# Optimization experiments

Measured on AMD Instinct MI355X. Metric: run time of the kernel, lower is better.

Reference implementation:

```python
import jax, jax.numpy as jnp
import numpy as np

N = 50000        # nodes
E = 800000       # edges (avg degree 16)
G = 64           # graphs in batch
F_IN = 9
OUT = 10


def setup_inputs() -> dict:
    key = jax.random.key(0)
    ks = jax.random.split(key, 20)
    def w(k, fi, fo):
        return jax.random.normal(k, (fi, fo), dtype=jnp.float32) * (1.0 / np.sqrt(fi))
    inp = {
        "x": jax.random.normal(ks[0], (N, F_IN), dtype=jnp.float32),
        "edge_index": jax.random.randint(ks[1], (2, E), 0, N, dtype=jnp.int64),
        "batch": jnp.sort(jax.random.randint(ks[2], (N,), 0, G, dtype=jnp.int64)),
        # GCNConv weights (PyG: x @ W then normalized scatter-add, + bias)
        "W1": w(ks[3], F_IN, 128), "b1": jnp.zeros((128,), jnp.float32),
        "W2": w(ks[4], 128, 256),  "b2": jnp.zeros((256,), jnp.float32),
        "W3": w(ks[5], 256, 256),  "b3": jnp.zeros((256,), jnp.float32),
        "W4": w(ks[6], 256, 256),  "b4": jnp.zeros((256,), jnp.float32),
        # dense head
        "Wl2": w(ks[7], 256, 128), "bl2": jnp.zeros((128,), jnp.float32),
        "Wl3": w(ks[8], 128, 128), "bl3": jnp.zeros((128,), jnp.float32),
        "Wl":  w(ks[9], 128, OUT), "bl":  jnp.zeros((OUT,), jnp.float32),
    }
    return inp


def reference(x, edge_index, batch, W1, b1, W2, b2, W3, b3, W4, b4,
              Wl2, bl2, Wl3, bl3, Wl, bl):
    # GCNConv with self-loops and symmetric deg^{-1/2} normalization
    loops = jnp.arange(N, dtype=edge_index.dtype)
    src = jnp.concatenate([edge_index[0], loops])   # [E+N]
    dst = jnp.concatenate([edge_index[1], loops])
    deg = jax.ops.segment_sum(jnp.ones_like(src, dtype=x.dtype), dst, num_segments=N)
    dinv = jax.lax.rsqrt(deg)                        # deg >= 1 due to self-loops
    norm = (dinv[src] * dinv[dst])[:, None]          # [E+N, 1]

    def conv(h, W, b):
        msg = (h @ W)[src] * norm                    # gather + normalize
        return jax.ops.segment_sum(msg, dst, num_segments=N) + b

    h = jax.nn.relu(conv(x, W1, b1))
    h = jax.nn.relu(conv(h, W2, b2))
    h = jax.nn.relu(conv(h, W3, b3))
    h = conv(h, W4, b4)                              # no relu before pool
    g = jax.ops.segment_max(h, batch, num_segments=G)  # global_max_pool -> [G, 256]
    g = jax.nn.relu(g @ Wl2 + bl2)
    g = jax.nn.relu(g @ Wl3 + bl3)
    out = g @ Wl + bl                                # [G, OUT]
    return jnp.squeeze(out)
```

## Files before the change

kernel.cpp:

```cpp
#include <hip/hip_runtime.h>
#include <float.h>

#define NN 50000
#define NE 800000
#define NG 64
#define CAP 64

typedef __attribute__((ext_vector_type(8))) short bf16x8;
typedef __attribute__((ext_vector_type(4))) float f32x4;
typedef __attribute__((ext_vector_type(4))) _Float16 half4;
typedef __attribute__((ext_vector_type(2))) _Float16 half2v;
typedef unsigned int u32;

__device__ __forceinline__ unsigned f2mono(float f) {
  unsigned b = __float_as_uint(f);
  return (b & 0x80000000u) ? ~b : (b | 0x80000000u);
}
__device__ __forceinline__ float mono2f(unsigned u) {
  unsigned b = (u & 0x80000000u) ? (u & 0x7fffffffu) : ~u;
  return __uint_as_float(b);
}
__device__ __forceinline__ unsigned short bf16rn(float f) {
  unsigned u = __float_as_uint(f);
  unsigned r = u + 0x7FFFu + ((u >> 16) & 1u);
  return (unsigned short)(r >> 16);
}
__device__ __forceinline__ float bf2f(unsigned short h) {
  return __uint_as_float(((unsigned)h) << 16);
}
__device__ __forceinline__ void split2(float a, unsigned short* hi, unsigned short* lo) {
  unsigned short h = bf16rn(a);
  *hi = h;
  *lo = bf16rn(a - bf2f(h));
}
__device__ __forceinline__ void gl_lds16(const void* g, void* l) {
  __builtin_amdgcn_global_load_lds((const __attribute__((address_space(1))) u32*)g,
                                   (__attribute__((address_space(3))) u32*)l, 16, 0, 0);
}

__global__ void k_count(const int* __restrict__ src, const int* __restrict__ dst,
                        int* __restrict__ cnt, int* __restrict__ col) {
  int e = blockIdx.x * blockDim.x + threadIdx.x;
  if (e >= NE) return;
  int d = dst[e];
  int s = src[e];
  if ((unsigned)d >= NN || (unsigned)s >= NN) return;
  int pos = atomicAdd(&cnt[d], 1);
  if (pos < CAP) col[d * CAP + pos] = s;
}

__global__ void k_dinv(const int* __restrict__ cnt, float* __restrict__ dinv,
                       const float* __restrict__ x, float* __restrict__ xs) {
  int v = blockIdx.x * blockDim.x + threadIdx.x;
  if (v >= NN) return;
  float d = rsqrtf((float)cnt[v] + 1.0f);
  dinv[v] = d;
#pragma unroll
  for (int i = 0; i < 9; ++i) xs[v * 9 + i] = x[v * 9 + i] * d;
}

__global__ void k_splitw(const float* __restrict__ W, unsigned short* __restrict__ Wi,
                         int K, int Nc) {
  int i = blockIdx.x * blockDim.x + threadIdx.x;
  if (i >= K * Nc) return;
  int k = i / Nc, n = i - k * Nc;
  float w = W[i];
  unsigned short h, l;
  split2(w, &h, &l);
  size_t base = (size_t)n * 2 * K + (size_t)(k >> 3) * 16 + (k & 7);
  Wi[base] = h;
  Wi[base + 8] = l;
}

__global__ __launch_bounds__(256) void k_agg9(const float* __restrict__ xs,
                                              float* __restrict__ out,
                                              const int* __restrict__ cnt,
                                              const int* __restrict__ col,
                                              const float* __restrict__ dinv) {
  int v = (blockIdx.x * 256 + threadIdx.x) >> 4;
  int l = threadIdx.x & 15;
  if (v >= NN) return;
  int c = cnt[v]; if (c > CAP) c = CAP;
  const int* cl = col + v * CAP;
  float acc = (l < 9) ? xs[v * 9 + l] : 0.0f;
  int j = 0;
  for (; j + 4 <= c; j += 4) {
    int4 u = *(const int4*)(cl + j);
    float a0 = (l < 9) ? xs[u.x * 9 + l] : 0.f;
    float a1 = (l < 9) ? xs[u.y * 9 + l] : 0.f;
    float a2 = (l < 9) ? xs[u.z * 9 + l] : 0.f;
    float a3 = (l < 9) ? xs[u.w * 9 + l] : 0.f;
    acc += (a0 + a1) + (a2 + a3);
  }
  for (; j < c; ++j) {
    int u = cl[j];
    if (l < 9) acc += xs[u * 9 + l];
  }
  if (l < 9) out[v * 9 + l] = acc * dinv[v];
}

__global__ __launch_bounds__(256) void k_gemm9(const float* __restrict__ in,
                                               const float* __restrict__ W,
                                               const float* __restrict__ bias,
                                               const float* __restrict__ dinv,
                                               _Float16* __restrict__ out) {
  __shared__ float sW[9 * 128];
  __shared__ float sb[128];
  int t = threadIdx.x;
  if (t < 128) sb[t] = bias[t];
  for (int i = t; i < 9 * 128; i += 256) sW[i] = W[i];
  __syncthreads();
  int r = blockIdx.x * 2 + (t >> 7);
  int c = t & 127;
  if (r >= NN) return;
  float acc = sb[c];
#pragma unroll
  for (int i = 0; i < 9; ++i) acc += in[r * 9 + i] * sW[i * 128 + c];
  out[r * 128 + c] = (_Float16)(fmaxf(acc, 0.0f) * dinv[r]);
}

__global__ __launch_bounds__(256) void k_agg128(const half2v* __restrict__ h,
                                                unsigned short* __restrict__ Ai,
                                                const int* __restrict__ cnt,
                                                const int* __restrict__ col,
                                                const float* __restrict__ dinv) {
  int w = (blockIdx.x * 256 + threadIdx.x) >> 6;
  int lane = threadIdx.x & 63;
  if (w >= NN) return;
  half2v s = h[(size_t)w * 64 + lane];
  float ax = (float)s.x, ay = (float)s.y;
  int c = cnt[w]; if (c > CAP) c = CAP;
  const int* cl = col + w * CAP;
  int j = 0;
  for (; j + 4 <= c; j += 4) {
    int4 u = *(const int4*)(cl + j);
    half2v t0 = h[(size_t)u.x * 64 + lane];
    half2v t1 = h[(size_t)u.y * 64 + lane];
    half2v t2 = h[(size_t)u.z * 64 + lane];
    half2v t3 = h[(size_t)u.w * 64 + lane];
    ax += ((float)t0.x + (float)t1.x) + ((float)t2.x + (float)t3.x);
    ay += ((float)t0.y + (float)t1.y) + ((float)t2.y + (float)t3.y);
  }
  for (; j < c; ++j) {
    int u = cl[j];
    half2v tv = h[(size_t)u * 64 + lane];
    ax += (float)tv.x; ay += (float)tv.y;
  }
  float di = dinv[w];
  ax *= di; ay *= di;
  ushort2 hv, lv;
  split2(ax, &hv.x, &lv.x);
  split2(ay, &hv.y, &lv.y);
  size_t base = (size_t)w * 256 + (size_t)(lane >> 2) * 16 + 2 * (lane & 3);
  *(ushort2*)(Ai + base) = hv;
  *(ushort2*)(Ai + base + 8) = lv;
}

__global__ __launch_bounds__(256) void k_agg256(const half4* __restrict__ h,
                                                unsigned short* __restrict__ Ai,
                                                const int* __restrict__ cnt,
                                                const int* __restrict__ col,
                                                const float* __restrict__ dinv) {
  int w = (blockIdx.x * 256 + threadIdx.x) >> 6;
  int lane = threadIdx.x & 63;
  if (w >= NN) return;
  half4 s = h[(size_t)w * 64 + lane];
  float ax = (float)s.x, ay = (float)s.y, az = (float)s.z, aw = (float)s.w;
  int c = cnt[w]; if (c > CAP) c = CAP;
  const int* cl = col + w * CAP;
  int j = 0;
  for (; j + 4 <= c; j += 4) {
    int4 u = *(const int4*)(cl + j);
    half4 t0 = h[(size_t)u.x * 64 + lane];
    half4 t1 = h[(size_t)u.y * 64 + lane];
    half4 t2 = h[(size_t)u.z * 64 + lane];
    half4 t3 = h[(size_t)u.w * 64 + lane];
    ax += ((float)t0.x + (float)t1.x) + ((float)t2.x + (float)t3.x);
    ay += ((float)t0.y + (float)t1.y) + ((float)t2.y + (float)t3.y);
    az += ((float)t0.z + (float)t1.z) + ((float)t2.z + (float)t3.z);
    aw += ((float)t0.w + (float)t1.w) + ((float)t2.w + (float)t3.w);
  }
  for (; j < c; ++j) {
    int u = cl[j];
    half4 tv = h[(size_t)u * 64 + lane];
    ax += (float)tv.x; ay += (float)tv.y; az += (float)tv.z; aw += (float)tv.w;
  }
  float di = dinv[w];
  ax *= di; ay *= di; az *= di; aw *= di;
  ushort4 hv, lv;
  split2(ax, &hv.x, &lv.x);
  split2(ay, &hv.y, &lv.y);
  split2(az, &hv.z, &lv.z);
  split2(aw, &hv.w, &lv.w);
  size_t base = (size_t)w * 512 + (size_t)(lane >> 1) * 16 + 4 * (lane & 1);
  *(ushort4*)(Ai + base) = hv;
  *(ushort4*)(Ai + base + 8) = lv;
}

__global__ __launch_bounds__(256) void k_mm(const unsigned short* __restrict__ A,
                                            const unsigned short* __restrict__ B,
                                            const float* __restrict__ bias,
                                            _Float16* __restrict__ C,
                                            const float* __restrict__ dinv,
                                            const int* __restrict__ batch,
                                            unsigned* __restrict__ gpool,
                                            int M, int K, int Nc, int mode) {
  __shared__ __align__(16) unsigned short Al[128 * 64];
  __shared__ __align__(16) unsigned short Bl[128 * 64];
  int t = threadIdx.x;
  int wave = t >> 6, lane = t & 63;
  int wm = wave & 1, wn = wave >> 1;
  int rowBase = blockIdx.x * 128;
  int colBase = blockIdx.y * 128;
  int lm = lane & 15;
  int q  = lane >> 4;
  unsigned K2 = 2u * (unsigned)K;

  int srl  = wave * 32 + (lane >> 3);
  int sj   = lane & 7;
  int ssw  = srl & 7;

  f32x4 acc[4][4];
#pragma unroll
  for (int i = 0; i < 4; ++i)
#pragma unroll
    for (int j = 0; j < 4; ++j) acc[i][j] = (f32x4){0.f, 0.f, 0.f, 0.f};

  int nsteps = K >> 5;
  for (int s = 0; s < nsteps; ++s) {
    __syncthreads();
#pragma unroll
    for (int c = 0; c < 4; ++c) {
      int rl = srl + c * 8;
      int gseg = s * 8 + (sj ^ ssw);
      int ga = rowBase + rl; if (ga > M - 1) ga = M - 1;
      gl_lds16(A + (size_t)ga * K2 + gseg * 8, Al + (wave * 32 + c * 8) * 64 + lane * 8);
      int gb = colBase + rl;
      gl_lds16(B + (size_t)gb * K2 + gseg * 8, Bl + (wave * 32 + c * 8) * 64 + lane * 8);
    }
    __syncthreads();

    bf16x8 bh[4], blv[4];
#pragma unroll
    for (int ni = 0; ni < 4; ++ni) {
      int r = wn * 64 + ni * 16 + lm;
      const unsigned short* p = Bl + r * 64;
      int sw = r & 7;
      bh[ni]  = *(const bf16x8*)(p + ((2 * q) ^ sw) * 8);
      blv[ni] = *(const bf16x8*)(p + ((2 * q + 1) ^ sw) * 8);
    }
#pragma unroll
    for (int mi = 0; mi < 4; ++mi) {
      int r = wm * 64 + mi * 16 + lm;
      const unsigned short* p = Al + r * 64;
      int sw = r & 7;
      bf16x8 ah = *(const bf16x8*)(p + ((2 * q) ^ sw) * 8);
      bf16x8 al = *(const bf16x8*)(p + ((2 * q + 1) ^ sw) * 8);
#pragma unroll
      for (int ni = 0; ni < 4; ++ni) {
        acc[mi][ni] = __builtin_amdgcn_mfma_f32_16x16x32_bf16(ah, bh[ni],  acc[mi][ni], 0, 0, 0);
        acc[mi][ni] = __builtin_amdgcn_mfma_f32_16x16x32_bf16(ah, blv[ni], acc[mi][ni], 0, 0, 0);
        acc[mi][ni] = __builtin_amdgcn_mfma_f32_16x16x32_bf16(al, bh[ni],  acc[mi][ni], 0, 0, 0);
      }
    }
  }

  int rowOff = (lane >> 4) * 4;
  if (mode == 2) {
    __syncthreads();
    unsigned* ldsPool = (unsigned*)Al;
    for (int i = t; i < 4 * 256; i += 256) ldsPool[i] = 0u;
    __syncthreads();
    int b0 = batch[rowBase];
#pragma unroll
    for (int mi = 0; mi < 4; ++mi) {
#pragma unroll
      for (int ni = 0; ni < 4; ++ni) {
        int gc = colBase + wn * 64 + ni * 16 + lm;
        float bsv = bias[gc];
#pragma unroll
        for (int r = 0; r < 4; ++r) {
          int gr = rowBase + wm * 64 + mi * 16 + rowOff + r;
          if (gr < M) {
            float v = acc[mi][ni][r] + bsv;
            int idx = batch[gr] - b0;
            if (idx < 0) idx = 0;
            if (idx > 3) idx = 3;
            atomicMax(&ldsPool[idx * 256 + gc], f2mono(v));
          }
        }
      }
    }
    __syncthreads();
#pragma unroll
    for (int s4 = 0; s4 < 4; ++s4) {
      unsigned mv = ldsPool[s4 * 256 + t];
      int gb = b0 + s4;
      if (mv && gb < NG) atomicMax(&gpool[gb * 256 + t], mv);
    }
  } else {
#pragma unroll
    for (int mi = 0; mi < 4; ++mi) {
#pragma unroll
      for (int ni = 0; ni < 4; ++ni) {
        int gc = colBase + wn * 64 + ni * 16 + lm;
        float bsv = bias[gc];
#pragma unroll
        for (int r = 0; r < 4; ++r) {
          int gr = rowBase + wm * 64 + mi * 16 + rowOff + r;
          if (gr < M) {
            float v = fmaxf(acc[mi][ni][r] + bsv, 0.0f);
            C[(size_t)gr * Nc + gc] = (_Float16)(v * dinv[gr]);
          }
        }
      }
    }
  }
}

__global__ __launch_bounds__(256) void k_head(const unsigned* __restrict__ g,
                                              const float* __restrict__ Wl2, const float* __restrict__ bl2,
                                              const float* __restrict__ Wl3, const float* __restrict__ bl3,
                                              const float* __restrict__ Wl, const float* __restrict__ bl,
                                              float* __restrict__ out) {
  __shared__ float s0[256];
  __shared__ float s1[128];
  __shared__ float s2[128];
  int b = blockIdx.x, t = threadIdx.x;
  s0[t] = mono2f(g[b * 256 + t]);
  __syncthreads();
  if (t < 128) {
    float acc = bl2[t];
    for (int k = 0; k < 256; ++k) acc += s0[k] * Wl2[k * 128 + t];
    s1[t] = fmaxf(acc, 0.0f);
  }
  __syncthreads();
  if (t < 128) {
    float acc = bl3[t];
    for (int k = 0; k < 128; ++k) acc += s1[k] * Wl3[k * 128 + t];
    s2[t] = fmaxf(acc, 0.0f);
  }
  __syncthreads();
  if (t < 10) {
    float acc = bl[t];
    for (int k = 0; k < 128; ++k) acc += s2[k] * Wl[k * 10 + t];
    out[b * 10 + t] = acc;
  }
}

extern "C" void kernel_launch(void* const* d_in, const int* in_sizes, int n_in,
                              void* d_out, int out_size, void* d_ws, size_t ws_size,
                              hipStream_t stream) {
  const float* x   = (const float*)d_in[0];
  const int* eidx  = (const int*)d_in[1];
  const int* batch = (const int*)d_in[2];
  const float* W1 = (const float*)d_in[3];   const float* b1 = (const float*)d_in[4];
  const float* W2 = (const float*)d_in[5];   const float* b2 = (const float*)d_in[6];
  const float* W3 = (const float*)d_in[7];   const float* b3 = (const float*)d_in[8];
  const float* W4 = (const float*)d_in[9];   const float* b4 = (const float*)d_in[10];
  const float* Wl2 = (const float*)d_in[11]; const float* bl2 = (const float*)d_in[12];
  const float* Wl3 = (const float*)d_in[13]; const float* bl3 = (const float*)d_in[14];
  const float* Wl  = (const float*)d_in[15]; const float* bl  = (const float*)d_in[16];
  float* out = (float*)d_out;

  _Float16* hs = (_Float16*)d_ws;
  unsigned short* Ai = (unsigned short*)(hs + (size_t)NN * 256);
  int* cnt  = (int*)(Ai + (size_t)NN * 512);
  float* dinv = (float*)(cnt + NN);
  int* col  = (int*)(dinv + NN);
  unsigned* g = (unsigned*)(col + (size_t)NN * CAP);
  unsigned short* W2i = (unsigned short*)(g + NG * 256);
  unsigned short* W3i = W2i + 256 * 256;
  unsigned short* W4i = W3i + 256 * 512;
  float* xs = (float*)hs;
  float* agg9out = (float*)Ai;

  const int* src = eidx;
  const int* dst = eidx + NE;

  hipMemsetAsync(cnt, 0, NN * sizeof(int), stream);
  hipMemsetAsync(g, 0, NG * 256 * sizeof(unsigned), stream);

  k_count<<<(NE + 255) / 256, 256, 0, stream>>>(src, dst, cnt, col);
  k_dinv<<<(NN + 255) / 256, 256, 0, stream>>>(cnt, dinv, x, xs);

  k_splitw<<<(128 * 256 + 255) / 256, 256, 0, stream>>>(W2, W2i, 128, 256);
  k_splitw<<<(256 * 256 + 255) / 256, 256, 0, stream>>>(W3, W3i, 256, 256);
  k_splitw<<<(256 * 256 + 255) / 256, 256, 0, stream>>>(W4, W4i, 256, 256);

  k_agg9<<<(NN + 15) / 16, 256, 0, stream>>>(xs, agg9out, cnt, col, dinv);
  k_gemm9<<<NN / 2, 256, 0, stream>>>(agg9out, W1, b1, dinv, hs);

  dim3 gmm((NN + 127) / 128, 2);

  k_agg128<<<(NN + 3) / 4, 256, 0, stream>>>((const half2v*)hs, Ai, cnt, col, dinv);
  k_mm<<<gmm, 256, 0, stream>>>(Ai, W2i, b2, hs, dinv, batch, g, NN, 128, 256, 1);

  k_agg256<<<(NN + 3) / 4, 256, 0, stream>>>((const half4*)hs, Ai, cnt, col, dinv);
  k_mm<<<gmm, 256, 0, stream>>>(Ai, W3i, b3, hs, dinv, batch, g, NN, 256, 256, 1);

  k_agg256<<<(NN + 3) / 4, 256, 0, stream>>>((const half4*)hs, Ai, cnt, col, dinv);
  k_mm<<<gmm, 256, 0, stream>>>(Ai, W4i, b4, hs, dinv, batch, g, NN, 256, 256, 2);

  k_head<<<NG, 256, 0, stream>>>(g, Wl2, bl2, Wl3, bl3, Wl, bl, out);
}
```

Baseline: 483.3 us.

## Replace bf16 split-3 GEMM with fp16 activations and split fp16 weights

```diff
diff --git a/kernel.cpp b/kernel.cpp
--- a/kernel.cpp
+++ b/kernel.cpp
@@ -6,7 +6,7 @@
 #define NG 64
 #define CAP 64
 
-typedef __attribute__((ext_vector_type(8))) short bf16x8;
+typedef __attribute__((ext_vector_type(8))) _Float16 f16x8;
 typedef __attribute__((ext_vector_type(4))) float f32x4;
 typedef __attribute__((ext_vector_type(4))) _Float16 half4;
 typedef __attribute__((ext_vector_type(2))) _Float16 half2v;
@@ -19,19 +19,6 @@
 __device__ __forceinline__ float mono2f(unsigned u) {
   unsigned b = (u & 0x80000000u) ? (u & 0x7fffffffu) : ~u;
   return __uint_as_float(b);
-}
-__device__ __forceinline__ unsigned short bf16rn(float f) {
-  unsigned u = __float_as_uint(f);
-  unsigned r = u + 0x7FFFu + ((u >> 16) & 1u);
-  return (unsigned short)(r >> 16);
-}
-__device__ __forceinline__ float bf2f(unsigned short h) {
-  return __uint_as_float(((unsigned)h) << 16);
-}
-__device__ __forceinline__ void split2(float a, unsigned short* hi, unsigned short* lo) {
-  unsigned short h = bf16rn(a);
-  *hi = h;
-  *lo = bf16rn(a - bf2f(h));
 }
 __device__ __forceinline__ void gl_lds16(const void* g, void* l) {
   __builtin_amdgcn_global_load_lds((const __attribute__((address_space(1))) u32*)g,
@@ -59,17 +46,16 @@
   for (int i = 0; i < 9; ++i) xs[v * 9 + i] = x[v * 9 + i] * d;
 }
 
-__global__ void k_splitw(const float* __restrict__ W, unsigned short* __restrict__ Wi,
-                         int K, int Nc) {
+__global__ void k_splitw(const float* __restrict__ W, _Float16* __restrict__ Wh,
+                         _Float16* __restrict__ Wl, int K, int Nc) {
   int i = blockIdx.x * blockDim.x + threadIdx.x;
   if (i >= K * Nc) return;
   int k = i / Nc, n = i - k * Nc;
   float w = W[i];
-  unsigned short h, l;
-  split2(w, &h, &l);
-  size_t base = (size_t)n * 2 * K + (size_t)(k >> 3) * 16 + (k & 7);
-  Wi[base] = h;
-  Wi[base + 8] = l;
+  _Float16 h = (_Float16)w;
+  _Float16 l = (_Float16)(w - (float)h);
+  Wh[(size_t)n * K + k] = h;
+  Wl[(size_t)n * K + k] = l;
 }
 
 __global__ __launch_bounds__(256) void k_agg9(const float* __restrict__ xs,
@@ -120,7 +106,7 @@
 }
 
 __global__ __launch_bounds__(256) void k_agg128(const half2v* __restrict__ h,
-                                                unsigned short* __restrict__ Ai,
+                                                half2v* __restrict__ out,
                                                 const int* __restrict__ cnt,
                                                 const int* __restrict__ col,
                                                 const float* __restrict__ dinv) {
@@ -147,17 +133,14 @@
     ax += (float)tv.x; ay += (float)tv.y;
   }
   float di = dinv[w];
-  ax *= di; ay *= di;
-  ushort2 hv, lv;
-  split2(ax, &hv.x, &lv.x);
-  split2(ay, &hv.y, &lv.y);
-  size_t base = (size_t)w * 256 + (size_t)(lane >> 2) * 16 + 2 * (lane & 3);
-  *(ushort2*)(Ai + base) = hv;
-  *(ushort2*)(Ai + base + 8) = lv;
+  half2v o;
+  o.x = (_Float16)(ax * di);
+  o.y = (_Float16)(ay * di);
+  out[(size_t)w * 64 + lane] = o;
 }
 
 __global__ __launch_bounds__(256) void k_agg256(const half4* __restrict__ h,
-                                                unsigned short* __restrict__ Ai,
+                                                half4* __restrict__ out,
                                                 const int* __restrict__ cnt,
                                                 const int* __restrict__ col,
                                                 const float* __restrict__ dinv) {
@@ -186,27 +169,26 @@
     ax += (float)tv.x; ay += (float)tv.y; az += (float)tv.z; aw += (float)tv.w;
   }
   float di = dinv[w];
-  ax *= di; ay *= di; az *= di; aw *= di;
-  ushort4 hv, lv;
-  split2(ax, &hv.x, &lv.x);
-  split2(ay, &hv.y, &lv.y);
-  split2(az, &hv.z, &lv.z);
-  split2(aw, &hv.w, &lv.w);
-  size_t base = (size_t)w * 512 + (size_t)(lane >> 1) * 16 + 4 * (lane & 1);
-  *(ushort4*)(Ai + base) = hv;
-  *(ushort4*)(Ai + base + 8) = lv;
-}
-
-__global__ __launch_bounds__(256) void k_mm(const unsigned short* __restrict__ A,
-                                            const unsigned short* __restrict__ B,
+  half4 o;
+  o.x = (_Float16)(ax * di);
+  o.y = (_Float16)(ay * di);
+  o.z = (_Float16)(az * di);
+  o.w = (_Float16)(aw * di);
+  out[(size_t)w * 64 + lane] = o;
+}
+
+__global__ __launch_bounds__(256) void k_mm(const _Float16* __restrict__ A,
+                                            const _Float16* __restrict__ Bh,
+                                            const _Float16* __restrict__ Bl,
                                             const float* __restrict__ bias,
                                             _Float16* __restrict__ C,
                                             const float* __restrict__ dinv,
                                             const int* __restrict__ batch,
                                             unsigned* __restrict__ gpool,
                                             int M, int K, int Nc, int mode) {
-  __shared__ __align__(16) unsigned short Al[128 * 64];
-  __shared__ __align__(16) unsigned short Bl[128 * 64];
+  __shared__ __align__(16) _Float16 Alds[128 * 64];
+  __shared__ __align__(16) _Float16 Bhl[128 * 64];
+  __shared__ __align__(16) _Float16 Bll[128 * 64];
   int t = threadIdx.x;
   int wave = t >> 6, lane = t & 63;
   int wm = wave & 1, wn = wave >> 1;
@@ -214,11 +196,11 @@
   int colBase = blockIdx.y * 128;
   int lm = lane & 15;
   int q  = lane >> 4;
-  unsigned K2 = 2u * (unsigned)K;
-
-  int srl  = wave * 32 + (lane >> 3);
-  int sj   = lane & 7;
-  int ssw  = srl & 7;
+
+  int srl = wave * 32 + (lane >> 3);
+  int sj  = lane & 7;
+  int ssw = lane >> 3;
+  int gseg = sj ^ ssw;
 
   f32x4 acc[4][4];
 #pragma unroll
@@ -226,41 +208,43 @@
 #pragma unroll
     for (int j = 0; j < 4; ++j) acc[i][j] = (f32x4){0.f, 0.f, 0.f, 0.f};
 
-  int nsteps = K >> 5;
-  for (int s = 0; s < nsteps; ++s) {
+  int nit = K >> 6;
+  for (int it = 0; it < nit; ++it) {
     __syncthreads();
 #pragma unroll
     for (int c = 0; c < 4; ++c) {
       int rl = srl + c * 8;
-      int gseg = s * 8 + (sj ^ ssw);
       int ga = rowBase + rl; if (ga > M - 1) ga = M - 1;
-      gl_lds16(A + (size_t)ga * K2 + gseg * 8, Al + (wave * 32 + c * 8) * 64 + lane * 8);
       int gb = colBase + rl;
-      gl_lds16(B + (size_t)gb * K2 + gseg * 8, Bl + (wave * 32 + c * 8) * 64 + lane * 8);
-    }
-    __syncthreads();
-
-    bf16x8 bh[4], blv[4];
-#pragma unroll
-    for (int ni = 0; ni < 4; ++ni) {
-      int r = wn * 64 + ni * 16 + lm;
-      const unsigned short* p = Bl + r * 64;
-      int sw = r & 7;
-      bh[ni]  = *(const bf16x8*)(p + ((2 * q) ^ sw) * 8);
-      blv[ni] = *(const bf16x8*)(p + ((2 * q + 1) ^ sw) * 8);
-    }
-#pragma unroll
-    for (int mi = 0; mi < 4; ++mi) {
-      int r = wm * 64 + mi * 16 + lm;
-      const unsigned short* p = Al + r * 64;
-      int sw = r & 7;
-      bf16x8 ah = *(const bf16x8*)(p + ((2 * q) ^ sw) * 8);
-      bf16x8 al = *(const bf16x8*)(p + ((2 * q + 1) ^ sw) * 8);
+      unsigned off = (unsigned)it * 64 + gseg * 8;
+      int ldst = (wave * 32 + c * 8) * 64 + lane * 8;
+      gl_lds16(A  + (size_t)ga * K + off, Alds + ldst);
+      gl_lds16(Bh + (size_t)gb * K + off, Bhl + ldst);
+      gl_lds16(Bl + (size_t)gb * K + off, Bll + ldst);
+    }
+    __syncthreads();
+
+#pragma unroll
+    for (int s2 = 0; s2 < 2; ++s2) {
+      int slotq = ((s2 << 2) | q);
+      f16x8 vbh[4], vbl[4];
 #pragma unroll
       for (int ni = 0; ni < 4; ++ni) {
-        acc[mi][ni] = __builtin_amdgcn_mfma_f32_16x16x32_bf16(ah, bh[ni],  acc[mi][ni], 0, 0, 0);
-        acc[mi][ni] = __builtin_amdgcn_mfma_f32_16x16x32_bf16(ah, blv[ni], acc[mi][ni], 0, 0, 0);
-        acc[mi][ni] = __builtin_amdgcn_mfma_f32_16x16x32_bf16(al, bh[ni],  acc[mi][ni], 0, 0, 0);
+        int rB = wn * 64 + ni * 16 + lm;
+        int slot = slotq ^ (lm & 7);
+        vbh[ni] = *(const f16x8*)(Bhl + rB * 64 + slot * 8);
+        vbl[ni] = *(const f16x8*)(Bll + rB * 64 + slot * 8);
+      }
+#pragma unroll
+      for (int mi = 0; mi < 4; ++mi) {
+        int rA = wm * 64 + mi * 16 + lm;
+        int slot = slotq ^ (lm & 7);
+        f16x8 va = *(const f16x8*)(Alds + rA * 64 + slot * 8);
+#pragma unroll
+        for (int ni = 0; ni < 4; ++ni) {
+          acc[mi][ni] = __builtin_amdgcn_mfma_f32_16x16x32_f16(va, vbh[ni], acc[mi][ni], 0, 0, 0);
+          acc[mi][ni] = __builtin_amdgcn_mfma_f32_16x16x32_f16(va, vbl[ni], acc[mi][ni], 0, 0, 0);
+        }
       }
     }
   }
@@ -268,7 +252,7 @@
   int rowOff = (lane >> 4) * 4;
   if (mode == 2) {
     __syncthreads();
-    unsigned* ldsPool = (unsigned*)Al;
+    unsigned* ldsPool = (unsigned*)Alds;
     for (int i = t; i < 4 * 256; i += 256) ldsPool[i] = 0u;
     __syncthreads();
     int b0 = batch[rowBase];
@@ -363,17 +347,20 @@
   const float* Wl  = (const float*)d_in[15]; const float* bl  = (const float*)d_in[16];
   float* out = (float*)d_out;
 
-  _Float16* hs = (_Float16*)d_ws;
-  unsigned short* Ai = (unsigned short*)(hs + (size_t)NN * 256);
-  int* cnt  = (int*)(Ai + (size_t)NN * 512);
+  _Float16* bufA = (_Float16*)d_ws;
+  _Float16* bufB = bufA + (size_t)NN * 256;
+  int* cnt  = (int*)(bufB + (size_t)NN * 256);
   float* dinv = (float*)(cnt + NN);
   int* col  = (int*)(dinv + NN);
   unsigned* g = (unsigned*)(col + (size_t)NN * CAP);
-  unsigned short* W2i = (unsigned short*)(g + NG * 256);
-  unsigned short* W3i = W2i + 256 * 256;
-  unsigned short* W4i = W3i + 256 * 512;
-  float* xs = (float*)hs;
-  float* agg9out = (float*)Ai;
+  _Float16* W2h = (_Float16*)(g + NG * 256);
+  _Float16* W2l = W2h + 256 * 128;
+  _Float16* W3h = W2l + 256 * 128;
+  _Float16* W3l = W3h + 256 * 256;
+  _Float16* W4h = W3l + 256 * 256;
+  _Float16* W4l = W4h + 256 * 256;
+  float* xs = (float*)bufA;
+  float* agg9out = (float*)bufB;
 
   const int* src = eidx;
   const int* dst = eidx + NE;
@@ -384,23 +371,23 @@
   k_count<<<(NE + 255) / 256, 256, 0, stream>>>(src, dst, cnt, col);
   k_dinv<<<(NN + 255) / 256, 256, 0, stream>>>(cnt, dinv, x, xs);
 
-  k_splitw<<<(128 * 256 + 255) / 256, 256, 0, stream>>>(W2, W2i, 128, 256);
-  k_splitw<<<(256 * 256 + 255) / 256, 256, 0, stream>>>(W3, W3i, 256, 256);
-  k_splitw<<<(256 * 256 + 255) / 256, 256, 0, stream>>>(W4, W4i, 256, 256);
+  k_splitw<<<(128 * 256 + 255) / 256, 256, 0, stream>>>(W2, W2h, W2l, 128, 256);
+  k_splitw<<<(256 * 256 + 255) / 256, 256, 0, stream>>>(W3, W3h, W3l, 256, 256);
+  k_splitw<<<(256 * 256 + 255) / 256, 256, 0, stream>>>(W4, W4h, W4l, 256, 256);
 
   k_agg9<<<(NN + 15) / 16, 256, 0, stream>>>(xs, agg9out, cnt, col, dinv);
-  k_gemm9<<<NN / 2, 256, 0, stream>>>(agg9out, W1, b1, dinv, hs);
+  k_gemm9<<<NN / 2, 256, 0, stream>>>(agg9out, W1, b1, dinv, bufA);
 
   dim3 gmm((NN + 127) / 128, 2);
 
-  k_agg128<<<(NN + 3) / 4, 256, 0, stream>>>((const half2v*)hs, Ai, cnt, col, dinv);
-  k_mm<<<gmm, 256, 0, stream>>>(Ai, W2i, b2, hs, dinv, batch, g, NN, 128, 256, 1);
-
-  k_agg256<<<(NN + 3) / 4, 256, 0, stream>>>((const half4*)hs, Ai, cnt, col, dinv);
-  k_mm<<<gmm, 256, 0, stream>>>(Ai, W3i, b3, hs, dinv, batch, g, NN, 256, 256, 1);
-
-  k_agg256<<<(NN + 3) / 4, 256, 0, stream>>>((const half4*)hs, Ai, cnt, col, dinv);
-  k_mm<<<gmm, 256, 0, stream>>>(Ai, W4i, b4, hs, dinv, batch, g, NN, 256, 256, 2);
+  k_agg128<<<(NN + 3) / 4, 256, 0, stream>>>((const half2v*)bufA, (half2v*)bufB, cnt, col, dinv);
+  k_mm<<<gmm, 256, 0, stream>>>(bufB, W2h, W2l, b2, bufA, dinv, batch, g, NN, 128, 256, 1);
+
+  k_agg256<<<(NN + 3) / 4, 256, 0, stream>>>((const half4*)bufA, (half4*)bufB, cnt, col, dinv);
+  k_mm<<<gmm, 256, 0, stream>>>(bufB, W3h, W3l, b3, bufA, dinv, batch, g, NN, 256, 256, 1);
+
+  k_agg256<<<(NN + 3) / 4, 256, 0, stream>>>((const half4*)bufA, (half4*)bufB, cnt, col, dinv);
+  k_mm<<<gmm, 256, 0, stream>>>(bufB, W4h, W4l, b4, bufA, dinv, batch, g, NN, 256, 256, 2);
 
   k_head<<<NG, 256, 0, stream>>>(g, Wl2, bl2, Wl3, bl3, Wl, bl, out);
 }
```

Result: faster. 455.0 us (-5.8%).
